# Kernel tuning notes

Measured on AMD Instinct MI355X. Metric: run time of the kernel, lower is better.

Reference implementation:

```python
import jax, jax.numpy as jnp
import numpy as np

WS = 8      # window size
NH = 8      # num heads
ED = 256    # embed dim
HD = ED // NH  # head dim


def conv2d(x, w, b):
    # x: [B,C,H,W], w: [O,I,3,3] (torch OIHW), SAME padding, stride 1
    y = jax.lax.conv_general_dilated(x, w, (1, 1), 'SAME',
                                     dimension_numbers=('NCHW', 'OIHW', 'NCHW'))
    return y + b[None, :, None, None]


def linear(x, w, b):
    # torch Linear: y = x @ W^T + b, w: [out,in]
    return jnp.einsum('bnc,oc->bno', x, w) + b


def window_partition(x, ws):
    B, C, H, W = x.shape
    x = x.reshape(B, C, H // ws, ws, W // ws, ws)
    x = jnp.transpose(x, (0, 2, 4, 3, 5, 1))  # B, H/ws, W/ws, ws, ws, C
    return x.reshape(-1, ws * ws, C)


def window_reverse(win, H, W, ws, C):
    nW = (H // ws) * (W // ws)
    B = win.shape[0] // nW
    x = win.reshape(B, H // ws, W // ws, ws, ws, C)
    x = jnp.transpose(x, (0, 5, 1, 3, 2, 4))
    return x.reshape(B, C, H, W)


def setup_inputs() -> dict:
    key = jax.random.key(0)
    ks = jax.random.split(key, 24)
    s = 0.02
    inp = {
        'xmap': jax.random.normal(ks[0], (4, ED, 256, 256), jnp.float32),
        'xfeat': jax.random.normal(ks[1], (4, 32, 256, 256), jnp.float32),
        'cmap_w': jax.random.normal(ks[2], (ED, ED, 3, 3), jnp.float32) * s,
        'cmap_b': jnp.zeros((ED,), jnp.float32),
        'cfeat_w': jax.random.normal(ks[3], (ED, 32, 3, 3), jnp.float32) * s,
        'cfeat_b': jnp.zeros((ED,), jnp.float32),
        'qxmap_w': jax.random.normal(ks[4], (ED, ED), jnp.float32) * s,
        'qxmap_b': jnp.zeros((ED,), jnp.float32),
        'kxmap_w': jax.random.normal(ks[5], (ED, ED), jnp.float32) * s,
        'kxmap_b': jnp.zeros((ED,), jnp.float32),
        'vxmap_w': jax.random.normal(ks[6], (ED, ED), jnp.float32) * s,
        'vxmap_b': jnp.zeros((ED,), jnp.float32),
        'qxfeat_w': jax.random.normal(ks[7], (ED, ED), jnp.float32) * s,
        'qxfeat_b': jnp.zeros((ED,), jnp.float32),
        'kxfeat_w': jax.random.normal(ks[8], (ED, ED), jnp.float32) * s,
        'kxfeat_b': jnp.zeros((ED,), jnp.float32),
        'proj_w': jax.random.normal(ks[9], (ED, ED), jnp.float32) * s,
        'proj_b': jnp.zeros((ED,), jnp.float32),
        'cout_w': jax.random.normal(ks[10], (ED, ED, 3, 3), jnp.float32) * s,
        'cout_b': jnp.zeros((ED,), jnp.float32),
    }
    return inp


def reference(xmap, xfeat, cmap_w, cmap_b, cfeat_w, cfeat_b,
              qxmap_w, qxmap_b, kxmap_w, kxmap_b, vxmap_w, vxmap_b,
              qxfeat_w, qxfeat_b, kxfeat_w, kxfeat_b,
              proj_w, proj_b, cout_w, cout_b):
    B, C, H, W = xmap.shape  # xfeat matches spatial size -> no interpolate branch
    xmap = conv2d(xmap, cmap_w, cmap_b)
    identity = xmap
    wm = window_partition(xmap, WS)                        # [Bw, N, C]
    wf = window_partition(conv2d(xfeat, cfeat_w, cfeat_b), WS)
    Bw, N, _ = wm.shape

    def heads(t):
        return jnp.transpose(t.reshape(Bw, N, NH, HD), (0, 2, 1, 3))  # [Bw,H,N,D]

    q_m = heads(linear(wm, qxmap_w, qxmap_b))
    k_m = heads(linear(wm, kxmap_w, kxmap_b))
    v_m = heads(linear(wm, vxmap_w, vxmap_b))
    q_f = heads(linear(wf, qxfeat_w, qxfeat_b))
    k_f = heads(linear(wf, kxfeat_w, kxfeat_b))

    q_g = jax.nn.sigmoid(q_f) * q_m
    k_g = jax.nn.sigmoid(k_f) * k_m

    scale = 1.0 / jnp.sqrt(jnp.asarray(HD, q_g.dtype))
    attn = jax.nn.softmax(jnp.einsum('bhnd,bhmd->bhnm', q_g, k_g) * scale, axis=-1)
    out = jnp.einsum('bhnm,bhmd->bhnd', attn, v_m)         # [Bw,H,N,D]
    out = jnp.transpose(out, (0, 2, 1, 3)).reshape(Bw, N, C)
    out = window_reverse(linear(out, proj_w, proj_b), H, W, WS, C)
    return conv2d(out, cout_w, cout_b) + identity
```

## Files before the change

kernel.cpp:

```cpp
#include <hip/hip_runtime.h>
#include <hip/hip_bf16.h>
#include <cstdint>
#include <math.h>

using bf16 = __hip_bfloat16;
typedef __attribute__((ext_vector_type(4))) float f32x4;
typedef __attribute__((ext_vector_type(8))) short s16x8;
typedef __attribute__((ext_vector_type(4))) short s16x4;

#define AS3(p) ((__attribute__((address_space(3))) void *)(p))
#define AS1(p) ((const __attribute__((address_space(1))) void *)(p))

static constexpr int Himg = 256, Wimg = 256, Bimg = 4;
static constexpr int HWimg = Himg * Wimg;
static constexpr int Ttok = Bimg * HWimg;

__device__ __forceinline__ void gld16(bf16* lds, const bf16* g) {
  __builtin_amdgcn_global_load_lds(AS1(g), AS3(lds), 16, 0, 0);
}

__device__ __forceinline__ unsigned short f2u(float f) {
  bf16 b = __float2bfloat16(f);
  unsigned short u; __builtin_memcpy(&u, &b, 2); return u;
}

__device__ __forceinline__ void remap_tile(int bid, int total, int NY, int BMv, int& t0, int& n0) {
  int lin = (bid & 7) * (total >> 3) + (bid >> 3);
  t0 = (lin / NY) * BMv;
  n0 = (lin % NY) * 128;
}

__global__ void k_zero4k(float* p) {
  p[blockIdx.x * 256 + threadIdx.x] = 0.f;
}

__global__ void k_castf2b(const float* __restrict__ s, bf16* __restrict__ d, int n) {
  int i = blockIdx.x * 256 + threadIdx.x;
  if (i < n) d[i] = __float2bfloat16(s[i]);
}

__global__ void k_copyf(const float* __restrict__ s, float* __restrict__ d, int n) {
  int i = blockIdx.x * 256 + threadIdx.x;
  if (i < n) d[i] = s[i];
}

__global__ void k_permconv(const float* __restrict__ w, bf16* __restrict__ o, int I) {
  int idx = blockIdx.x * 256 + threadIdx.x;
  int tot = 256 * 9 * I;
  if (idx >= tot) return;
  int i   = idx % I;
  int rem = idx / I;
  int tap = rem % 9;
  int oc  = rem / 9;
  o[idx] = __float2bfloat16(w[(oc * I + i) * 9 + tap]);
}

__global__ void k_tohwc(const float* __restrict__ src, bf16* __restrict__ dst, int C) {
  int bh = blockIdx.x;
  int w0 = blockIdx.y * 32;
  int c0 = blockIdx.z * 32;
  int b = bh / Himg, h = bh % Himg;
  __shared__ float tile[32][33];
  int tid = threadIdx.x;
  int x = tid & 31, y = tid >> 5;
  const float* sp = src + (size_t)b * C * HWimg + (size_t)h * Wimg;
#pragma unroll
  for (int p = 0; p < 4; ++p) {
    int cl = y + p * 8;
    tile[cl][x] = sp[(size_t)(c0 + cl) * HWimg + w0 + x];
  }
  __syncthreads();
#pragma unroll
  for (int p = 0; p < 4; ++p) {
    int wl = y + p * 8;
    dst[((size_t)bh * Wimg + w0 + wl) * C + c0 + x] = __float2bfloat16(tile[x][wl]);
  }
}

__global__ void k_tochw(const bf16* __restrict__ src, float* __restrict__ dst) {
  int bh = blockIdx.x, w0 = blockIdx.y * 32, c0 = blockIdx.z * 32;
  int b = bh >> 8, h = bh & 255;
  __shared__ float tile[32][33];
  int tid = threadIdx.x, x = tid & 31, y = tid >> 5;
  const bf16* sp = src + (size_t)bh * Wimg * 256;
#pragma unroll
  for (int p = 0; p < 4; ++p) {
    int wl = y + p * 8;
    tile[wl][x] = __bfloat162float(sp[(size_t)(w0 + wl) * 256 + c0 + x]);
  }
  __syncthreads();
#pragma unroll
  for (int p = 0; p < 4; ++p) {
    int cl = y + p * 8;
    dst[(((size_t)b * 256 + c0 + cl) * Himg + h) * Wimg + w0 + x] = tile[x][cl];
  }
}

template <int CIN, int TAPS, int EPI>
__global__ void __launch_bounds__(256, 2)
k_gemm(const bf16* __restrict__ Ain, const bf16* __restrict__ BT,
       const float* __restrict__ bias,
       bf16* __restrict__ outb, int ldo,
       const bf16* __restrict__ ident,
       const bf16* __restrict__ zp, int NY)
{
  constexpr int KTOT = TAPS * CIN;
  constexpr int NK = KTOT / 32;
  int t0, n0;
  remap_tile(blockIdx.x, gridDim.x, NY, 256, t0, n0);
  const int tid = threadIdx.x;
  const int wave = tid >> 6, lane = tid & 63;
  const int seg = lane & 3;
  const int rr  = lane >> 2;

  __shared__ bf16 sA0[256 * 32];
  __shared__ bf16 sA1[256 * 32];
  __shared__ bf16 sA2[256 * 32];
  __shared__ bf16 sB0[128 * 32];
  __shared__ bf16 sB1[128 * 32];
  __shared__ bf16 sB2[128 * 32];

  f32x4 acc[8][4] = {};

  const int wr = wave >> 1, wc = wave & 1;
  const int fr = lane & 15, fq = lane >> 4;
  const int sseg = (seg ^ ((rr >> 1) & 3)) * 8;
  const int slot = (fq ^ ((fr >> 1) & 3)) * 8;

#define STAGE(WA, WB, KSV) do {                                                 \
    const int k0_ = (KSV) * 32;                                                 \
    const int tap_ = k0_ / CIN;                                                 \
    const int c0_ = k0_ - tap_ * CIN;                                           \
    const int dy_ = tap_ / 3 - 1, dx_ = tap_ % 3 - 1;                           \
    _Pragma("unroll") for (int i_ = 0; i_ < 4; ++i_) {                          \
      const int g_ = i_ * 4 + wave;                                             \
      const int t_ = t0 + g_ * 16 + rr;                                         \
      const bf16* src_;                                                         \
      if (TAPS == 1) {                                                          \
        src_ = Ain + (size_t)t_ * CIN + k0_ + sseg;                             \
      } else {                                                                  \
        const int hh_ = ((t_ >> 8) & 255) + dy_, ww_ = (t_ & 255) + dx_;        \
        const bool v_ = ((unsigned)hh_ < 256u) && ((unsigned)ww_ < 256u);       \
        const long gi_ = (long)t_ + dy_ * Wimg + dx_;                           \
        src_ = v_ ? (Ain + gi_ * CIN + c0_ + sseg) : (zp + sseg);               \
      }                                                                         \
      gld16(WA + g_ * 16 * 32, src_);                                           \
    }                                                                           \
    _Pragma("unroll") for (int i_ = 0; i_ < 2; ++i_) {                          \
      const int g_ = i_ * 4 + wave;                                             \
      gld16(WB + g_ * 16 * 32,                                                  \
            BT + (size_t)(n0 + g_ * 16 + rr) * KTOT + k0_ + sseg);              \
    }                                                                           \
  } while (0)

#define GSTEP(RA, RB, WA, WB, KSV, LASTF) do {                                  \
    if (LASTF) { asm volatile("s_waitcnt vmcnt(0)" ::: "memory"); }             \
    else       { asm volatile("s_waitcnt vmcnt(6)" ::: "memory"); }             \
    __builtin_amdgcn_s_barrier();                                               \
    s16x8 af_[8], bf_[4];                                                       \
    _Pragma("unroll") for (int m_ = 0; m_ < 8; ++m_)                            \
      af_[m_] = *(const s16x8*)(RA + (wr * 128 + m_ * 16 + fr) * 32 + slot);    \
    _Pragma("unroll") for (int n_ = 0; n_ < 4; ++n_)                            \
      bf_[n_] = *(const s16x8*)(RB + (wc * 64 + n_ * 16 + fr) * 32 + slot);     \
    if ((KSV) + 2 < NK) STAGE(WA, WB, (KSV) + 2);                               \
    __builtin_amdgcn_s_setprio(1);                                              \
    _Pragma("unroll") for (int m_ = 0; m_ < 8; ++m_)                            \
      _Pragma("unroll") for (int n_ = 0; n_ < 4; ++n_)                          \
        acc[m_][n_] = __builtin_amdgcn_mfma_f32_16x16x32_bf16(af_[m_], bf_[n_], acc[m_][n_], 0, 0, 0); \
    __builtin_amdgcn_s_setprio(0);                                              \
  } while (0)

  STAGE(sA0, sB0, 0);
  STAGE(sA1, sB1, 1);

  constexpr int NMAIN = ((NK - 1) / 3) * 3;
  int ks = 0;
#pragma unroll 1
  for (; ks < NMAIN; ks += 3) {
    GSTEP(sA0, sB0, sA2, sB2, ks,     false);
    GSTEP(sA1, sB1, sA0, sB0, ks + 1, false);
    GSTEP(sA2, sB2, sA1, sB1, ks + 2, false);
  }
  constexpr int TREM = NK - NMAIN;
  if constexpr (TREM == 3) {
    GSTEP(sA0, sB0, sA2, sB2, NMAIN,     false);
    GSTEP(sA1, sB1, sA0, sB0, NMAIN + 1, false);
    GSTEP(sA2, sB2, sA1, sB1, NMAIN + 2, true);
  } else if constexpr (TREM == 2) {
    GSTEP(sA0, sB0, sA2, sB2, NMAIN,     false);
    GSTEP(sA1, sB1, sA0, sB0, NMAIN + 1, true);
  } else {
    GSTEP(sA0, sB0, sA2, sB2, NMAIN,     true);
  }
#undef GSTEP
#undef STAGE

#pragma unroll
  for (int m = 0; m < 8; ++m) {
#pragma unroll
    for (int n = 0; n < 4; ++n) {
      const int col = n0 + wc * 64 + n * 16 + fr;
#pragma unroll
      for (int j = 0; j < 4; ++j) {
        const int row = wr * 128 + m * 16 + fq * 4 + j;
        const size_t t = (size_t)t0 + row;
        float v = acc[m][n][j] + bias[col];
        if (EPI == 0) {
          outb[t * ldo + col] = __float2bfloat16(v);
        } else {
          v += __bfloat162float(ident[t * 256 + col]);
          outb[t * 256 + col] = __float2bfloat16(v);
        }
      }
    }
  }
}

__global__ void __launch_bounds__(256, 2)
k_gemm_qkv(const bf16* __restrict__ Am, const bf16* __restrict__ Af,
           const bf16* __restrict__ Bm, const bf16* __restrict__ Bf,
           const float* __restrict__ bm, const float* __restrict__ bfi,
           bf16* __restrict__ out)
{
  int t0, n0;
  remap_tile(blockIdx.x, gridDim.x, 4, 128, t0, n0);
  const int tid = threadIdx.x;
  const int wave = tid >> 6, lane = tid & 63;
  const int seg = lane & 3;
  const int rr  = lane >> 2;

  __shared__ bf16 sA0[128 * 32];
  __shared__ bf16 sA1[128 * 32];
  __shared__ bf16 sA2[128 * 32];
  __shared__ bf16 sB0[128 * 32];
  __shared__ bf16 sB1[128 * 32];
  __shared__ bf16 sB2[128 * 32];

  f32x4 accm[4][4] = {};
  f32x4 accf[4][4] = {};

  const int wr = wave >> 1, wc = wave & 1;
  const int fr = lane & 15, fq = lane >> 4;
  const int sseg = (seg ^ ((rr >> 1) & 3)) * 8;
  const int slot = (fq ^ ((fr >> 1) & 3)) * 8;

#define STAGEQ(WA, WB, SV) do {                                                 \
    const int k0_ = ((SV) >> 1) * 32;                                           \
    const bf16* A_ = ((SV) & 1) ? Af : Am;                                      \
    const bf16* B_ = ((SV) & 1) ? Bf : Bm;                                      \
    _Pragma("unroll") for (int i_ = 0; i_ < 2; ++i_) {                          \
      const int r_ = wave * 32 + i_ * 16 + rr;                                  \
      gld16(WA + (wave * 32 + i_ * 16) * 32, A_ + (size_t)(t0 + r_) * 256 + k0_ + sseg); \
      gld16(WB + (wave * 32 + i_ * 16) * 32, B_ + (size_t)(n0 + r_) * 256 + k0_ + sseg); \
    }                                                                           \
  } while (0)

#define QSTEP(RA, RB, WA, WB, SV, LASTF) do {                                   \
    if (LASTF) { asm volatile("s_waitcnt vmcnt(0)" ::: "memory"); }             \
    else       { asm volatile("s_waitcnt vmcnt(4)" ::: "memory"); }             \
    __builtin_amdgcn_s_barrier();                                               \
    s16x8 af_[4], bf_[4];                                                       \
    _Pragma("unroll") for (int m_ = 0; m_ < 4; ++m_)                            \
      af_[m_] = *(const s16x8*)(RA + (wr * 64 + m_ * 16 + fr) * 32 + slot);     \
    _Pragma("unroll") for (int n_ = 0; n_ < 4; ++n_)                            \
      bf_[n_] = *(const s16x8*)(RB + (wc * 64 + n_ * 16 + fr) * 32 + slot);     \
    if ((SV) + 2 < 16) STAGEQ(WA, WB, (SV) + 2);                                \
    __builtin_amdgcn_s_setprio(1);                                              \
    if ((SV) & 1) {                                                             \
      _Pragma("unroll") for (int m_ = 0; m_ < 4; ++m_)                          \
        _Pragma("unroll") for (int n_ = 0; n_ < 4; ++n_)                        \
          accf[m_][n_] = __builtin_amdgcn_mfma_f32_16x16x32_bf16(af_[m_], bf_[n_], accf[m_][n_], 0, 0, 0); \
    } else {                                                                    \
      _Pragma("unroll") for (int m_ = 0; m_ < 4; ++m_)                          \
        _Pragma("unroll") for (int n_ = 0; n_ < 4; ++n_)                        \
          accm[m_][n_] = __builtin_amdgcn_mfma_f32_16x16x32_bf16(af_[m_], bf_[n_], accm[m_][n_], 0, 0, 0); \
    }                                                                           \
    __builtin_amdgcn_s_setprio(0);                                              \
  } while (0)

  STAGEQ(sA0, sB0, 0);
  STAGEQ(sA1, sB1, 1);

  int s = 0;
#pragma unroll 1
  for (; s < 15; s += 3) {
    QSTEP(sA0, sB0, sA2, sB2, s,     false);
    QSTEP(sA1, sB1, sA0, sB0, s + 1, false);
    QSTEP(sA2, sB2, sA1, sB1, s + 2, false);
  }
  QSTEP(sA0, sB0, sA2, sB2, 15, true);
#undef QSTEP
#undef STAGEQ

#pragma unroll
  for (int m = 0; m < 4; ++m) {
#pragma unroll
    for (int n = 0; n < 4; ++n) {
      const int col = n0 + wc * 64 + n * 16 + fr;
#pragma unroll
      for (int j = 0; j < 4; ++j) {
        const int row = wr * 64 + m * 16 + fq * 4 + j;
        const size_t t = (size_t)t0 + row;
        float v = accm[m][n][j] + bm[col];
        const float g = accf[m][n][j] + bfi[col];
        v *= 1.f / (1.f + __expf(-g));
        out[t * 768 + col] = __float2bfloat16(v);
      }
    }
  }
}

__global__ void __launch_bounds__(256, 2)
k_attn_mfma(const bf16* __restrict__ qkv, bf16* __restrict__ out) {
  __shared__ short smem[4 * 7424];
  const int tid = threadIdx.x;
  const int wave = tid >> 6, lane = tid & 63;
  const int fr = lane & 15, fq = lane >> 4;
  const int wi = blockIdx.x >> 1;
  const int head = (blockIdx.x & 1) * 4 + wave;
  const int b = wi >> 10, rem = wi & 1023, wh = rem >> 5, ww = rem & 31;
  const size_t tbase = (size_t)b * HWimg + (size_t)(wh * 8) * Wimg + ww * 8;

  short* Qs = smem + wave * 7424;
  short* Ks = Qs + 2560;
  short* VT = Qs + 5120;
  short* P  = Qs;
  short* Ol = Qs;

  auto tok = [&](int i) -> size_t {
    return tbase + (size_t)(i >> 3) * Wimg + (i & 7);
  };

  {
    const bf16* tb = qkv + tok(lane) * 768 + head * 32;
#pragma unroll
    for (int c = 0; c < 4; ++c) {
      s16x8 qv = *(const s16x8*)(tb + c * 8);
      s16x8 kv = *(const s16x8*)(tb + 256 + c * 8);
      s16x8 vv = *(const s16x8*)(tb + 512 + c * 8);
      *(s16x8*)(Qs + lane * 40 + c * 8) = qv;
      *(s16x8*)(Ks + lane * 40 + c * 8) = kv;
#pragma unroll
      for (int e = 0; e < 8; ++e) VT[(c * 8 + e) * 72 + lane] = vv[e];
    }
  }

  s16x8 kf[4], qf[4];
#pragma unroll
  for (int m = 0; m < 4; ++m)
    kf[m] = *(const s16x8*)(Ks + (fr + 16 * m) * 40 + fq * 8);
#pragma unroll
  for (int n = 0; n < 4; ++n)
    qf[n] = *(const s16x8*)(Qs + (fr + 16 * n) * 40 + fq * 8);

  f32x4 st[4][4] = {};
#pragma unroll
  for (int m = 0; m < 4; ++m)
#pragma unroll
    for (int n = 0; n < 4; ++n)
      st[m][n] = __builtin_amdgcn_mfma_f32_16x16x32_bf16(kf[m], qf[n], st[m][n], 0, 0, 0);

  const float scale = 0.17677669529663688f;
  float invs[4];
#pragma unroll
  for (int n = 0; n < 4; ++n) {
    float mx = -1e30f;
#pragma unroll
    for (int m = 0; m < 4; ++m)
#pragma unroll
      for (int j = 0; j < 4; ++j) mx = fmaxf(mx, st[m][n][j]);
    mx = fmaxf(mx, __shfl_xor(mx, 16));
    mx = fmaxf(mx, __shfl_xor(mx, 32));
    float sum = 0.f;
#pragma unroll
    for (int m = 0; m < 4; ++m) {
      s16x4 pk;
#pragma unroll
      for (int j = 0; j < 4; ++j) {
        float e = __expf((st[m][n][j] - mx) * scale);
        sum += e;
        pk[j] = (short)f2u(e);
      }
      *(s16x4*)(P + (fr + 16 * n) * 72 + 16 * m + 4 * fq) = pk;
    }
    sum += __shfl_xor(sum, 16);
    sum += __shfl_xor(sum, 32);
    invs[n] = 1.f / sum;
  }

  f32x4 oc[4][2] = {};
#pragma unroll
  for (int ks = 0; ks < 2; ++ks) {
    s16x8 pf[4], vf[2];
#pragma unroll
    for (int m = 0; m < 4; ++m)
      pf[m] = *(const s16x8*)(P + (fr + 16 * m) * 72 + ks * 32 + fq * 8);
#pragma unroll
    for (int n = 0; n < 2; ++n)
      vf[n] = *(const s16x8*)(VT + (fr + 16 * n) * 72 + ks * 32 + fq * 8);
#pragma unroll
    for (int m = 0; m < 4; ++m)
#pragma unroll
      for (int n = 0; n < 2; ++n)
        oc[m][n] = __builtin_amdgcn_mfma_f32_16x16x32_bf16(pf[m], vf[n], oc[m][n], 0, 0, 0);
  }

#pragma unroll
  for (int m = 0; m < 4; ++m)
#pragma unroll
    for (int j = 0; j < 4; ++j) {
      const float inv = __shfl(invs[m], 4 * fq + j);
      const int q = 16 * m + 4 * fq + j;
#pragma unroll
      for (int n = 0; n < 2; ++n)
        Ol[q * 40 + fr + 16 * n] = (short)f2u(oc[m][n][j] * inv);
    }
  {
    bf16* op = out + tok(lane) * 256 + head * 32;
#pragma unroll
    for (int c = 0; c < 4; ++c)
      *(s16x8*)(op + c * 8) = *(const s16x8*)(Ol + lane * 40 + c * 8);
  }
}

extern "C" void kernel_launch(void* const* d_in, const int* in_sizes, int n_in,
                              void* d_out, int out_size, void* d_ws, size_t ws_size,
                              hipStream_t stream) {
  const float* xmap    = (const float*)d_in[0];
  const float* xfeat   = (const float*)d_in[1];
  const float* cmap_w  = (const float*)d_in[2];
  const float* cmap_b  = (const float*)d_in[3];
  const float* cfeat_w = (const float*)d_in[4];
  const float* cfeat_b = (const float*)d_in[5];
  const float* qxmap_w = (const float*)d_in[6];
  const float* qxmap_b = (const float*)d_in[7];
  const float* kxmap_w = (const float*)d_in[8];
  const float* kxmap_b = (const float*)d_in[9];
  const float* vxmap_w = (const float*)d_in[10];
  const float* vxmap_b = (const float*)d_in[11];
  const float* qxfeat_w = (const float*)d_in[12];
  const float* qxfeat_b = (const float*)d_in[13];
  const float* kxfeat_w = (const float*)d_in[14];
  const float* kxfeat_b = (const float*)d_in[15];
  const float* proj_w  = (const float*)d_in[16];
  const float* proj_b  = (const float*)d_in[17];
  const float* cout_w  = (const float*)d_in[18];
  const float* cout_b  = (const float*)d_in[19];

  uint8_t* ws = (uint8_t*)d_ws;
  size_t off = 0;
  auto alloc = [&](size_t bytes) -> void* {
    void* p = ws + off;
    off += (bytes + 255) & ~(size_t)255;
    return p;
  };
  float* zp       = (float*)alloc(4096);
  bf16* cmap_wT   = (bf16*)alloc((size_t)2304 * 256 * 2);
  bf16* cout_wT   = (bf16*)alloc((size_t)2304 * 256 * 2);
  bf16* cfeat_wT  = (bf16*)alloc((size_t)288 * 256 * 2);
  bf16* lin_qkv_wT= (bf16*)alloc((size_t)768 * 256 * 2);
  bf16* lin_f_wT  = (bf16*)alloc((size_t)512 * 256 * 2);
  bf16* proj_wT   = (bf16*)alloc((size_t)256 * 256 * 2);
  float* bias_qkv = (float*)alloc(768 * 4);
  float* bias_f   = (float*)alloc(512 * 4);
  bf16* xm_nhwc   = (bf16*)alloc((size_t)Ttok * 256 * 2);
  bf16* xf_nhwc   = (bf16*)alloc((size_t)Ttok * 32 * 2);
  bf16* xc        = (bf16*)alloc((size_t)Ttok * 256 * 2);
  bf16* fc        = (bf16*)alloc((size_t)Ttok * 256 * 2);
  bf16* qkv       = (bf16*)alloc((size_t)Ttok * 768 * 2);
  bf16* attn_out  = xm_nhwc;
  bf16* proj_out  = fc;
  bf16* convout   = qkv;
  bf16* zpb = (bf16*)zp;

  k_zero4k<<<4, 256, 0, stream>>>(zp);
  k_permconv<<<(256 * 9 * 256 + 255) / 256, 256, 0, stream>>>(cmap_w, cmap_wT, 256);
  k_permconv<<<(256 * 9 * 256 + 255) / 256, 256, 0, stream>>>(cout_w, cout_wT, 256);
  k_permconv<<<(256 * 9 * 32 + 255) / 256, 256, 0, stream>>>(cfeat_w, cfeat_wT, 32);
  k_castf2b<<<256, 256, 0, stream>>>(qxmap_w, lin_qkv_wT, 65536);
  k_castf2b<<<256, 256, 0, stream>>>(kxmap_w, lin_qkv_wT + 65536, 65536);
  k_castf2b<<<256, 256, 0, stream>>>(vxmap_w, lin_qkv_wT + 131072, 65536);
  k_castf2b<<<256, 256, 0, stream>>>(qxfeat_w, lin_f_wT, 65536);
  k_castf2b<<<256, 256, 0, stream>>>(kxfeat_w, lin_f_wT + 65536, 65536);
  k_castf2b<<<256, 256, 0, stream>>>(proj_w, proj_wT, 65536);
  k_copyf<<<1, 256, 0, stream>>>(qxmap_b, bias_qkv, 256);
  k_copyf<<<1, 256, 0, stream>>>(kxmap_b, bias_qkv + 256, 256);
  k_copyf<<<1, 256, 0, stream>>>(vxmap_b, bias_qkv + 512, 256);
  k_copyf<<<1, 256, 0, stream>>>(qxfeat_b, bias_f, 256);
  k_copyf<<<1, 256, 0, stream>>>(kxfeat_b, bias_f + 256, 256);

  k_tohwc<<<dim3(Bimg * Himg, Wimg / 32, 256 / 32), 256, 0, stream>>>(xmap, xm_nhwc, 256);
  k_tohwc<<<dim3(Bimg * Himg, Wimg / 32, 1), 256, 0, stream>>>(xfeat, xf_nhwc, 32);

  dim3 blk(256);
  const int NT256 = Ttok / 256;
  k_gemm<256, 9, 0><<<dim3(NT256 * 2), blk, 0, stream>>>(
      xm_nhwc, cmap_wT, cmap_b, xc, 256, nullptr, zpb, 2);
  k_gemm<32, 9, 0><<<dim3(NT256 * 2), blk, 0, stream>>>(
      xf_nhwc, cfeat_wT, cfeat_b, fc, 256, nullptr, zpb, 2);
  k_gemm<256, 1, 0><<<dim3(NT256 * 2), blk, 0, stream>>>(
      xc, lin_qkv_wT + 131072, bias_qkv + 512, qkv + 512, 768, nullptr, zpb, 2);
  k_gemm_qkv<<<dim3((Ttok / 128) * 4), blk, 0, stream>>>(
      xc, fc, lin_qkv_wT, lin_f_wT, bias_qkv, bias_f, qkv);
  k_attn_mfma<<<dim3(4096 * 2), blk, 0, stream>>>(qkv, attn_out);
  k_gemm<256, 1, 0><<<dim3(NT256 * 2), blk, 0, stream>>>(
      attn_out, proj_wT, proj_b, proj_out, 256, nullptr, zpb, 2);
  k_gemm<256, 9, 2><<<dim3(NT256 * 2), blk, 0, stream>>>(
      proj_out, cout_wT, cout_b, convout, 256, xc, zpb, 2);
  k_tochw<<<dim3(Bimg * Himg, Wimg / 32, 256 / 32), 256, 0, stream>>>(convout, (float*)d_out);
}
```

Measured before the change: 1.556 ms.

## Add 8-wave 256x256-tile GEMM with double-buffered LDS pipeline for 256-channel convs/linears

Introduces k_gemm8, a 512-thread kernel that computes a full 256x256 output tile per block instead of two 256x128 tiles. It uses four-way split LDS buffers, global_load_lds prefetch interleaved with MFMA phases, explicit vmcnt waits, barriers and setprio. The 3x3 convs with 256 input channels, the V linear and the proj linear now use it. The goal is to halve redundant A-tile loads and overlap memory with compute. In exchange it uses 128 KB of LDS at one block per CU with a large accumulator register file, so occupancy drops.

```diff
diff --git a/kernel.cpp b/kernel.cpp
--- a/kernel.cpp
+++ b/kernel.cpp
@@ -24,8 +24,11 @@
   unsigned short u; __builtin_memcpy(&u, &b, 2); return u;
 }
 
+__device__ __forceinline__ int remap_lin(int bid, int total) {
+  return (bid & 7) * (total >> 3) + (bid >> 3);
+}
 __device__ __forceinline__ void remap_tile(int bid, int total, int NY, int BMv, int& t0, int& n0) {
-  int lin = (bid & 7) * (total >> 3) + (bid >> 3);
+  int lin = remap_lin(bid, total);
   t0 = (lin / NY) * BMv;
   n0 = (lin % NY) * 128;
 }
@@ -93,6 +96,153 @@
   for (int p = 0; p < 4; ++p) {
     int cl = y + p * 8;
     dst[(((size_t)b * 256 + c0 + cl) * Himg + h) * Wimg + w0 + x] = tile[x][cl];
+  }
+}
+
+template <int TAPS, int EPI>
+__global__ void __launch_bounds__(512, 1)
+k_gemm8(const bf16* __restrict__ Ain, const bf16* __restrict__ BT,
+        const float* __restrict__ bias,
+        bf16* __restrict__ outb, int ldo,
+        const bf16* __restrict__ ident,
+        const bf16* __restrict__ zp)
+{
+  constexpr int KTOT = TAPS * 256;
+  constexpr int NK64 = KTOT / 64;
+  constexpr int NI   = NK64 / 2;
+  const int t0 = remap_lin(blockIdx.x, gridDim.x) * 256;
+  const int tid  = threadIdx.x;
+  const int wave = tid >> 6, lane = tid & 63;
+  const int wr = wave >> 2, wc = wave & 3;
+  const int fr = lane & 15, fq = lane >> 4;
+
+  __shared__ bf16 A0k0[256 * 32];
+  __shared__ bf16 A0k1[256 * 32];
+  __shared__ bf16 A1k0[256 * 32];
+  __shared__ bf16 A1k1[256 * 32];
+  __shared__ bf16 B0k0[256 * 32];
+  __shared__ bf16 B0k1[256 * 32];
+  __shared__ bf16 B1k0[256 * 32];
+  __shared__ bf16 B1k1[256 * 32];
+
+  f32x4 acc[8][4] = {};
+  s16x8 bfr[4];
+
+  const int slot8 = (fq ^ ((fr >> 1) & 3)) * 8;
+  const int aoff  = (wr * 128 + fr) * 32 + slot8;
+  const int boff  = (wc * 64 + fr) * 32 + slot8;
+  const int ldsl  = (tid & 3) * 8;
+  const int scol  = ((tid & 3) ^ ((tid >> 3) & 3)) * 8;
+  const int srow  = tid >> 2;
+
+#define STA(DST, KT, U) do {                                                     \
+    const int k0_ = (KT) * 64 + (U) * 32;                                        \
+    const int tap_ = k0_ >> 8;                                                   \
+    const int c0_ = k0_ & 255;                                                   \
+    const int dy_ = tap_ / 3 - 1, dx_ = tap_ % 3 - 1;                            \
+    _Pragma("unroll") for (int j_ = 0; j_ < 2; ++j_) {                           \
+      const int r_ = j_ * 128 + srow;                                            \
+      const int t_ = t0 + r_;                                                    \
+      const bf16* s_;                                                            \
+      if (TAPS == 1) {                                                           \
+        s_ = Ain + (size_t)t_ * 256 + k0_ + scol;                                \
+      } else {                                                                   \
+        const int hh_ = ((t_ >> 8) & 255) + dy_, ww_ = (t_ & 255) + dx_;         \
+        const bool v_ = ((unsigned)hh_ < 256u) && ((unsigned)ww_ < 256u);        \
+        const long gi_ = (long)t_ + dy_ * Wimg + dx_;                            \
+        s_ = v_ ? (Ain + gi_ * 256 + c0_ + scol) : (zp + scol);                  \
+      }                                                                          \
+      gld16(DST + r_ * 32 + ldsl, s_);                                           \
+    }                                                                            \
+  } while (0)
+
+#define STB(DST, KT, U) do {                                                     \
+    const int k0_ = (KT) * 64 + (U) * 32;                                        \
+    _Pragma("unroll") for (int j_ = 0; j_ < 2; ++j_) {                           \
+      const int ch_ = j_ * 128 + srow;                                           \
+      gld16(DST + ch_ * 32 + ldsl, BT + (size_t)ch_ * KTOT + k0_ + scol);        \
+    }                                                                            \
+  } while (0)
+
+#define NVM
+#define VM4 asm volatile("s_waitcnt vmcnt(4)" ::: "memory")
+#define VM0 asm volatile("s_waitcnt vmcnt(0)" ::: "memory")
+
+#define PH(RA, RB, MH, READB, VMSTMT, ...) do {                                  \
+    s16x8 af_[4];                                                                \
+    _Pragma("unroll") for (int q_ = 0; q_ < 4; ++q_)                             \
+      af_[q_] = *(const s16x8*)((RA) + aoff + ((MH) * 4 + q_) * 512);            \
+    if (READB) {                                                                 \
+      _Pragma("unroll") for (int n_ = 0; n_ < 4; ++n_)                           \
+        bfr[n_] = *(const s16x8*)((RB) + boff + n_ * 512);                       \
+    }                                                                            \
+    __VA_ARGS__;                                                                 \
+    __builtin_amdgcn_s_barrier();                                                \
+    asm volatile("s_waitcnt lgkmcnt(0)" ::: "memory");                           \
+    __builtin_amdgcn_sched_barrier(0);                                           \
+    __builtin_amdgcn_s_setprio(1);                                               \
+    _Pragma("unroll") for (int q_ = 0; q_ < 4; ++q_)                             \
+      _Pragma("unroll") for (int n_ = 0; n_ < 4; ++n_)                           \
+        acc[(MH) * 4 + q_][n_] = __builtin_amdgcn_mfma_f32_16x16x32_bf16(        \
+            af_[q_], bfr[n_], acc[(MH) * 4 + q_][n_], 0, 0, 0);                  \
+    __builtin_amdgcn_s_setprio(0);                                               \
+    VMSTMT;                                                                      \
+    __builtin_amdgcn_s_barrier();                                                \
+  } while (0)
+
+  STA(A0k0, 0, 0); STB(B0k0, 0, 0);
+  STA(A0k1, 0, 1); STB(B0k1, 0, 1);
+  VM4;
+  __builtin_amdgcn_s_barrier();
+
+#pragma unroll 1
+  for (int i = 0; i < NI - 1; ++i) {
+    const int v = 2 * i + 1, w = 2 * i + 2;
+    PH(A0k0, B0k0, 0, 1, NVM, STA(A1k0, v, 0));
+    PH(A0k0, B0k0, 1, 0, VM4, STB(B1k0, v, 0));
+    PH(A0k1, B0k1, 0, 1, NVM, STA(A1k1, v, 1));
+    PH(A0k1, B0k1, 1, 0, VM4, STB(B1k1, v, 1));
+    PH(A1k0, B1k0, 0, 1, NVM, STA(A0k0, w, 0));
+    PH(A1k0, B1k0, 1, 0, VM4, STB(B0k0, w, 0));
+    PH(A1k1, B1k1, 0, 1, NVM, STA(A0k1, w, 1));
+    PH(A1k1, B1k1, 1, 0, VM4, STB(B0k1, w, 1));
+  }
+  {
+    const int v = 2 * NI - 1;
+    PH(A0k0, B0k0, 0, 1, NVM, STA(A1k0, v, 0));
+    PH(A0k0, B0k0, 1, 0, VM4, STB(B1k0, v, 0));
+    PH(A0k1, B0k1, 0, 1, NVM, STA(A1k1, v, 1));
+    PH(A0k1, B0k1, 1, 0, VM4, STB(B1k1, v, 1));
+    PH(A1k0, B1k0, 0, 1, NVM, );
+    PH(A1k0, B1k0, 1, 0, VM0, );
+    PH(A1k1, B1k1, 0, 1, NVM, );
+    PH(A1k1, B1k1, 1, 0, NVM, );
+  }
+#undef PH
+#undef STA
+#undef STB
+#undef NVM
+#undef VM4
+#undef VM0
+
+#pragma unroll
+  for (int m = 0; m < 8; ++m) {
+#pragma unroll
+    for (int n = 0; n < 4; ++n) {
+      const int col = wc * 64 + n * 16 + fr;
+#pragma unroll
+      for (int j = 0; j < 4; ++j) {
+        const int row = wr * 128 + m * 16 + fq * 4 + j;
+        const size_t t = (size_t)t0 + row;
+        float v = acc[m][n][j] + bias[col];
+        if (EPI == 0) {
+          outb[t * ldo + col] = __float2bfloat16(v);
+        } else {
+          v += __bfloat162float(ident[t * 256 + col]);
+          outb[t * 256 + col] = __float2bfloat16(v);
+        }
+      }
+    }
   }
 }
 
@@ -492,20 +642,19 @@
   k_tohwc<<<dim3(Bimg * Himg, Wimg / 32, 256 / 32), 256, 0, stream>>>(xmap, xm_nhwc, 256);
   k_tohwc<<<dim3(Bimg * Himg, Wimg / 32, 1), 256, 0, stream>>>(xfeat, xf_nhwc, 32);
 
-  dim3 blk(256);
-  const int NT256 = Ttok / 256;
-  k_gemm<256, 9, 0><<<dim3(NT256 * 2), blk, 0, stream>>>(
-      xm_nhwc, cmap_wT, cmap_b, xc, 256, nullptr, zpb, 2);
-  k_gemm<32, 9, 0><<<dim3(NT256 * 2), blk, 0, stream>>>(
+  const int NB = Ttok / 256;
+  k_gemm8<9, 0><<<dim3(NB), dim3(512), 0, stream>>>(
+      xm_nhwc, cmap_wT, cmap_b, xc, 256, nullptr, zpb);
+  k_gemm<32, 9, 0><<<dim3(NB * 2), dim3(256), 0, stream>>>(
       xf_nhwc, cfeat_wT, cfeat_b, fc, 256, nullptr, zpb, 2);
-  k_gemm<256, 1, 0><<<dim3(NT256 * 2), blk, 0, stream>>>(
-      xc, lin_qkv_wT + 131072, bias_qkv + 512, qkv + 512, 768, nullptr, zpb, 2);
-  k_gemm_qkv<<<dim3((Ttok / 128) * 4), blk, 0, stream>>>(
+  k_gemm8<1, 0><<<dim3(NB), dim3(512), 0, stream>>>(
+      xc, lin_qkv_wT + 131072, bias_qkv + 512, qkv + 512, 768, nullptr, zpb);
+  k_gemm_qkv<<<dim3((Ttok / 128) * 4), dim3(256), 0, stream>>>(
       xc, fc, lin_qkv_wT, lin_f_wT, bias_qkv, bias_f, qkv);
-  k_attn_mfma<<<dim3(4096 * 2), blk, 0, stream>>>(qkv, attn_out);
-  k_gemm<256, 1, 0><<<dim3(NT256 * 2), blk, 0, stream>>>(
-      attn_out, proj_wT, proj_b, proj_out, 256, nullptr, zpb, 2);
-  k_gemm<256, 9, 2><<<dim3(NT256 * 2), blk, 0, stream>>>(
-      proj_out, cout_wT, cout_b, convout, 256, xc, zpb, 2);
+  k_attn_mfma<<<dim3(4096 * 2), dim3(256), 0, stream>>>(qkv, attn_out);
+  k_gemm8<1, 0><<<dim3(NB), dim3(512), 0, stream>>>(
+      attn_out, proj_wT, proj_b, proj_out, 256, nullptr, zpb);
+  k_gemm8<9, 2><<<dim3(NB), dim3(512), 0, stream>>>(
+      proj_out, cout_wT, cout_b, convout, 256, xc, zpb);
   k_tochw<<<dim3(Bimg * Himg, Wimg / 32, 256 / 32), 256, 0, stream>>>(convout, (float*)d_out);
 }
```

After: 1.576 ms. No clear change (+1.2%).
